# Optimization experiments

Measured on AMD Instinct MI355X. Metric: run time of the kernel, lower is better.

Reference implementation:

```python
import jax, jax.numpy as jnp
import numpy as np


def setup_inputs() -> dict:
    key = jax.random.key(0)
    kq, kk, kv = jax.random.split(key, 3)
    B, L, S, H, E = 4, 2048, 2048, 16, 64
    queries = jax.random.normal(kq, (B, L, H, E), dtype=jnp.float32)
    keys = jax.random.normal(kk, (B, S, H, E), dtype=jnp.float32)
    values = jax.random.normal(kv, (B, S, H, E), dtype=jnp.float32)
    return {"queries": queries, "keys": keys, "values": values}


def reference(queries, keys, values):
    # queries: [b,l,h,e], keys: [b,s,h,e], values: [b,s,h,d]
    e = queries.shape[-1]
    scale = 1.0 / jnp.sqrt(jnp.asarray(e, dtype=queries.dtype))
    scores = jnp.einsum('blhe,bshe->bhls', queries, keys)  # [b,h,l,s]
    attn_map = jax.nn.softmax(scale * scores, axis=-1)
    # dropout is identity in eval/reference mode
    v = jnp.einsum('bhls,bshd->blhd', attn_map, values)  # [b,l,h,d]
    return v, attn_map
```

## Files before the change

kernel.cpp:

```cpp
#include <hip/hip_runtime.h>
#include <hip/hip_bf16.h>


typedef __attribute__((ext_vector_type(4)))  float  f32x4;
typedef __attribute__((ext_vector_type(8)))  short  short8;
typedef __attribute__((ext_vector_type(4)))  short  short4v;
typedef __attribute__((ext_vector_type(4)))  unsigned short u16x4;

__device__ __forceinline__ unsigned short bf(float x) {
  return __builtin_bit_cast(unsigned short, __float2bfloat16(x));
}

__device__ __forceinline__ float bf2f(unsigned short u) {
  return __builtin_bit_cast(float, (unsigned int)u << 16);
}

__device__ __forceinline__ unsigned short f2bf(float f) {
  unsigned int u = __builtin_bit_cast(unsigned int, f);
  return (unsigned short)((u + 0x7FFFu + ((u >> 16) & 1u)) >> 16);
}

#define MFMA16(A, Bv, C) __builtin_amdgcn_mfma_f32_16x16x32_bf16(A, Bv, C, 0, 0, 0)


__global__ __launch_bounds__(256) void conv_all(const float* __restrict__ Q,
                                                const float* __restrict__ K,
                                                const float* __restrict__ V,
                                                unsigned short* __restrict__ Qbf,
                                                unsigned short* __restrict__ Kbf,
                                                unsigned short* __restrict__ VTbf) {
  __shared__ unsigned short T[64][68];
  if (blockIdx.x < 8192) {
    int idx = blockIdx.x * 256 + threadIdx.x;
    int isK = idx >> 20;
    int rem = idx & 0xFFFFF;
    int e0 = (rem & 7) << 3;
    int h  = (rem >> 3) & 15;
    int l  = (rem >> 7) & 2047;
    int b  = rem >> 18;
    const float* src = (isK ? K : Q) + (((size_t)(b * 2048 + l)) * 16 + h) * 64 + e0;
    unsigned short* dst = (isK ? Kbf : Qbf) + (((size_t)(b * 16 + h)) * 2048 + l) * 64 + e0;
    float sc = isK ? 1.0f : 0.18033688011112042f;
    float4 a = *(const float4*)src;
    float4 c = *(const float4*)(src + 4);
    u16x4 o0 = { bf(a.x * sc), bf(a.y * sc), bf(a.z * sc), bf(a.w * sc) };
    u16x4 o1 = { bf(c.x * sc), bf(c.y * sc), bf(c.z * sc), bf(c.w * sc) };
    *(u16x4*)dst = o0;
    *(u16x4*)(dst + 4) = o1;
  } else {
    int bid = blockIdx.x - 8192;
    int sc = bid & 31, bh = bid >> 5;
    int h = bh & 15, b = bh >> 4;
    int t = threadIdx.x;
    int srow = t >> 2, d0 = (t & 3) << 4;
    const float* src = V + (((size_t)(b * 2048 + sc * 64 + srow)) * 16 + h) * 64 + d0;
    float4 v0 = *(const float4*)(src + 0);
    float4 v1 = *(const float4*)(src + 4);
    float4 v2 = *(const float4*)(src + 8);
    float4 v3 = *(const float4*)(src + 12);
    T[d0+ 0][srow]=bf(v0.x); T[d0+ 1][srow]=bf(v0.y); T[d0+ 2][srow]=bf(v0.z); T[d0+ 3][srow]=bf(v0.w);
    T[d0+ 4][srow]=bf(v1.x); T[d0+ 5][srow]=bf(v1.y); T[d0+ 6][srow]=bf(v1.z); T[d0+ 7][srow]=bf(v1.w);
    T[d0+ 8][srow]=bf(v2.x); T[d0+ 9][srow]=bf(v2.y); T[d0+10][srow]=bf(v2.z); T[d0+11][srow]=bf(v2.w);
    T[d0+12][srow]=bf(v3.x); T[d0+13][srow]=bf(v3.y); T[d0+14][srow]=bf(v3.z); T[d0+15][srow]=bf(v3.w);
    __syncthreads();
    int d = t >> 2, s0 = (t & 3) << 4;
    unsigned short* dst = VTbf + ((size_t)bh * 64 + d) * 2048 + sc * 64 + s0;
#pragma unroll
    for (int j = 0; j < 16; j += 4) {
      u16x4 x = { T[d][s0 + j], T[d][s0 + j + 1], T[d][s0 + j + 2], T[d][s0 + j + 3] };
      *(u16x4*)(dst + j) = x;
    }
  }
}


__device__ __forceinline__ void gll16(const void* g, void* l) {
  __builtin_amdgcn_global_load_lds(
      (const __attribute__((address_space(1))) unsigned int*)g,
      (__attribute__((address_space(3))) unsigned int*)l, 16, 0, 0);
}

__device__ __forceinline__ void stage16(const unsigned short* gsrc, int rowStride,
                                        unsigned short* dstRow0, int lane) {
  int rr = lane >> 3;
  int cc = ((lane & 7) ^ rr) << 3;
  gll16(gsrc + (size_t)rr * rowStride + cc,       dstRow0);
  gll16(gsrc + (size_t)(8 + rr) * rowStride + cc, dstRow0 + 8 * 64);
}

__device__ __forceinline__ short8 frag(const unsigned short* tile, int row, int colb) {
  return *(const short8*)((const char*)tile + row * 128 + (colb ^ ((row & 7) << 4)));
}

__global__ __launch_bounds__(256, 3) void attn_main(
    const unsigned short* __restrict__ Qbf, const unsigned short* __restrict__ Kbf,
    const unsigned short* __restrict__ VTbf, float* __restrict__ Og,
    float* __restrict__ Ag) {

  int wg = ((blockIdx.x & 7) << 8) | (blockIdx.x >> 3);
  int qt = wg & 31, bh = wg >> 5;
  int h = bh & 15, b = bh >> 4;

  int tid = threadIdx.x, lane = tid & 63, w = tid >> 6;
  int g = lane >> 4, r16 = lane & 15;

  __shared__ __align__(16) unsigned short Qb[64][64];
  __shared__ __align__(16) unsigned short Kb[2][64][64];
  __shared__ __align__(16) unsigned short Vb[2][64][64];
  __shared__ __align__(16) unsigned short Pb[4][16][72];

  const unsigned short* qg = Qbf + ((size_t)bh * 2048 + qt * 64 + w * 16) * 64;
  const unsigned short* kg = Kbf + (size_t)bh * 2048 * 64 + (size_t)(w * 16) * 64;
  const unsigned short* vg = VTbf + (size_t)bh * 64 * 2048 + (size_t)(w * 16) * 2048;

  stage16(qg, 64, &Qb[w * 16][0], lane);
  stage16(kg,            64, &Kb[0][w * 16][0], lane);
  stage16(kg + 4096,     64, &Kb[1][w * 16][0], lane);
  stage16(kg + 2 * 4096, 64, &Vb[0][w * 16][0], lane);
  stage16(kg + 3 * 4096, 64, &Vb[1][w * 16][0], lane);
  asm volatile("s_waitcnt vmcnt(8)" ::: "memory");
  __builtin_amdgcn_s_barrier();

  short8 qf0 = frag(&Qb[0][0], w * 16 + r16, g * 16);
  short8 qf1 = frag(&Qb[0][0], w * 16 + r16, 64 + g * 16);

  float lsum = 0.0f;
  for (int ii = 0; ii < 16; ++ii) {
    const int hi = ii & 1;
    const unsigned short* sA = hi ? &Vb[0][0][0] : &Kb[0][0][0];
    const unsigned short* sB = hi ? &Vb[1][0][0] : &Kb[1][0][0];

    if (ii < 15) {
      asm volatile("s_waitcnt vmcnt(4)" ::: "memory");
    } else {
      asm volatile("s_waitcnt vmcnt(0)" ::: "memory");
    }
    __builtin_amdgcn_s_barrier();

    f32x4 st[8];
    __builtin_amdgcn_s_setprio(1);
#pragma unroll
    for (int t = 0; t < 4; ++t) {
      short8 kf0 = frag(sA, t * 16 + r16, g * 16);
      short8 kf1 = frag(sA, t * 16 + r16, 64 + g * 16);
      f32x4 z = {0.f, 0.f, 0.f, 0.f};
      z = MFMA16(kf0, qf0, z);
      z = MFMA16(kf1, qf1, z);
      st[t] = z;
    }
#pragma unroll
    for (int t = 0; t < 4; ++t) {
      short8 kf0 = frag(sB, t * 16 + r16, g * 16);
      short8 kf1 = frag(sB, t * 16 + r16, 64 + g * 16);
      f32x4 z = {0.f, 0.f, 0.f, 0.f};
      z = MFMA16(kf0, qf0, z);
      z = MFMA16(kf1, qf1, z);
      st[t + 4] = z;
    }
    __builtin_amdgcn_s_setprio(0);

    float acc = 0.f;
#pragma unroll
    for (int t = 0; t < 8; ++t) {
      float e0 = __builtin_amdgcn_exp2f(st[t][0]) + __builtin_amdgcn_exp2f(st[t][1]);
      float e1 = __builtin_amdgcn_exp2f(st[t][2]) + __builtin_amdgcn_exp2f(st[t][3]);
      acc += e0 + e1;
    }
    lsum += acc;

    __builtin_amdgcn_s_barrier();

    if (ii < 14) {
      const unsigned short* nk = kg + (size_t)(2 * ii + 4) * 4096;
      unsigned short* dA = hi ? &Vb[0][w * 16][0] : &Kb[0][w * 16][0];
      unsigned short* dB = hi ? &Vb[1][w * 16][0] : &Kb[1][w * 16][0];
      stage16(nk,        64, dA, lane);
      stage16(nk + 4096, 64, dB, lane);
    }
  }
  lsum += __shfl_xor(lsum, 16, 64);
  lsum += __shfl_xor(lsum, 32, 64);
  float rinv = 1.0f / lsum;

  f32x4 oacc[4];
#pragma unroll
  for (int t = 0; t < 4; ++t) oacc[t] = (f32x4){0.f, 0.f, 0.f, 0.f};

  stage16(kg, 64, &Kb[0][w * 16][0], lane);
  stage16(vg, 2048, &Vb[0][w * 16][0], lane);
  asm volatile("s_waitcnt vmcnt(0)" ::: "memory");
  __builtin_amdgcn_s_barrier();
  int cur = 0;

  float* aW = Ag + ((size_t)bh * 2048 + (size_t)(qt * 64 + w * 16)) * 2048;
  const int sra = lane >> 4;
  const int src4 = (lane & 15) * 4;

  for (int ch = 0; ch < 32; ++ch) {
    if (ch < 31) {
      stage16(kg + (size_t)(ch + 1) * 4096, 64, &Kb[cur ^ 1][w * 16][0], lane);
      stage16(vg + (size_t)(ch + 1) * 64, 2048, &Vb[cur ^ 1][w * 16][0], lane);
    }
    f32x4 st[4];
    __builtin_amdgcn_s_setprio(1);
#pragma unroll
    for (int t = 0; t < 4; ++t) {
      short8 kf0 = frag(&Kb[cur][0][0], t * 16 + r16, g * 16);
      short8 kf1 = frag(&Kb[cur][0][0], t * 16 + r16, 64 + g * 16);
      f32x4 z = {0.f, 0.f, 0.f, 0.f};
      z = MFMA16(kf0, qf0, z);
      z = MFMA16(kf1, qf1, z);
      st[t] = z;
    }
    __builtin_amdgcn_s_setprio(0);

#pragma unroll
    for (int t = 0; t < 4; ++t) {
      f32x4 p;
#pragma unroll
      for (int r = 0; r < 4; ++r)
        p[r] = __builtin_amdgcn_exp2f(st[t][r]) * rinv;
      u16x4 pb = { bf(p[0]), bf(p[1]), bf(p[2]), bf(p[3]) };
      *(u16x4*)&Pb[w][r16][t * 16 + 4 * g] = pb;
    }

#pragma unroll
    for (int i = 0; i < 4; ++i) {
      int row = 4 * i + sra;
      u16x4 pb4 = *(const u16x4*)&Pb[w][row][src4];
      f32x4 o = { bf2f(pb4[0]), bf2f(pb4[1]), bf2f(pb4[2]), bf2f(pb4[3]) };
      __builtin_nontemporal_store(o, (f32x4*)(aW + (size_t)row * 2048 + ch * 64 + src4));
    }

    __builtin_amdgcn_s_setprio(1);
#pragma unroll
    for (int c = 0; c < 2; ++c) {
      short8 pa = *(const short8*)((const char*)&Pb[w][r16][0] + c * 64 + g * 16);
#pragma unroll
      for (int t = 0; t < 4; ++t) {
        short8 vf = frag(&Vb[cur][0][0], t * 16 + r16, c * 64 + g * 16);
        oacc[t] = MFMA16(pa, vf, oacc[t]);
      }
    }
    __builtin_amdgcn_s_setprio(0);

    asm volatile("s_waitcnt vmcnt(4)" ::: "memory");
    __builtin_amdgcn_s_barrier();
    cur ^= 1;
  }

  float* op = Og + (((size_t)b * 2048 + (size_t)(qt * 64 + w * 16 + 4 * g)) * 16 + h) * 64;
#pragma unroll
  for (int t = 0; t < 4; ++t)
#pragma unroll
    for (int r = 0; r < 4; ++r)
      op[(size_t)r * 1024 + t * 16 + r16] = oacc[t][r];
}


__global__ __launch_bounds__(256, 2) void attn_fused(
    const float* __restrict__ Qg, const float* __restrict__ Kg,
    const float* __restrict__ Vg, float* __restrict__ Og,
    float* __restrict__ Ag) {

  const int qt = blockIdx.x & 31;
  const int bh = blockIdx.x >> 5;
  const int h  = bh & 15;
  const int b  = bh >> 4;

  const int tid  = threadIdx.x;
  const int lane = tid & 63;
  const int w    = tid >> 6;
  const int g    = lane >> 4;
  const int r16  = lane & 15;

  __shared__ __align__(16) unsigned short Qbuf[64][72];
  __shared__ __align__(16) unsigned short Kbuf[64][72];
  __shared__ __align__(16) unsigned short VT[64][68];
  __shared__ __align__(16) unsigned short Pbuf[4][16][72];

  const size_t inbase = (size_t)b * (2048u * 1024u) + (size_t)h * 64u;
  const int q0 = qt << 6;

  const int srow = tid >> 2;
  const int sd0  = (tid & 3) << 4;

  {
    const float sc = 0.18033688011112042f;
    const float* gp = Qg + inbase + (size_t)(q0 + srow) * 1024u + sd0;
    float4 va = *(const float4*)(gp + 0);
    float4 vb = *(const float4*)(gp + 4);
    float4 vc = *(const float4*)(gp + 8);
    float4 vd = *(const float4*)(gp + 12);
    unsigned short* dst = &Qbuf[srow][sd0];
    dst[0]=f2bf(va.x*sc); dst[1]=f2bf(va.y*sc); dst[2]=f2bf(va.z*sc); dst[3]=f2bf(va.w*sc);
    dst[4]=f2bf(vb.x*sc); dst[5]=f2bf(vb.y*sc); dst[6]=f2bf(vb.z*sc); dst[7]=f2bf(vb.w*sc);
    dst[8]=f2bf(vc.x*sc); dst[9]=f2bf(vc.y*sc); dst[10]=f2bf(vc.z*sc); dst[11]=f2bf(vc.w*sc);
    dst[12]=f2bf(vd.x*sc); dst[13]=f2bf(vd.y*sc); dst[14]=f2bf(vd.z*sc); dst[15]=f2bf(vd.w*sc);
  }
  __syncthreads();

  const short8 qf0 = *(const short8*)&Qbuf[w*16 + r16][g*8];
  const short8 qf1 = *(const short8*)&Qbuf[w*16 + r16][32 + g*8];

  f32x4 mrow = { -3e38f, -3e38f, -3e38f, -3e38f };
  f32x4 lrow = { 0.f, 0.f, 0.f, 0.f };

  for (int ch = 0; ch < 32; ++ch) {
    __syncthreads();
    {
      const float* gp = Kg + inbase + (size_t)(ch*64 + srow) * 1024u + sd0;
      float4 va = *(const float4*)(gp + 0);
      float4 vb = *(const float4*)(gp + 4);
      float4 vc = *(const float4*)(gp + 8);
      float4 vd = *(const float4*)(gp + 12);
      unsigned short* dst = &Kbuf[srow][sd0];
      dst[0]=f2bf(va.x); dst[1]=f2bf(va.y); dst[2]=f2bf(va.z); dst[3]=f2bf(va.w);
      dst[4]=f2bf(vb.x); dst[5]=f2bf(vb.y); dst[6]=f2bf(vb.z); dst[7]=f2bf(vb.w);
      dst[8]=f2bf(vc.x); dst[9]=f2bf(vc.y); dst[10]=f2bf(vc.z); dst[11]=f2bf(vc.w);
      dst[12]=f2bf(vd.x); dst[13]=f2bf(vd.y); dst[14]=f2bf(vd.z); dst[15]=f2bf(vd.w);
    }
    __syncthreads();

    f32x4 st[4];
#pragma unroll
    for (int t = 0; t < 4; ++t) {
      const short8 kf0 = *(const short8*)&Kbuf[t*16 + r16][g*8];
      const short8 kf1 = *(const short8*)&Kbuf[t*16 + r16][32 + g*8];
      f32x4 z = {0.f, 0.f, 0.f, 0.f};
      z = MFMA16(qf0, kf0, z);
      z = MFMA16(qf1, kf1, z);
      st[t] = z;
    }

    f32x4 cm = st[0];
#pragma unroll
    for (int t = 1; t < 4; ++t)
#pragma unroll
      for (int r = 0; r < 4; ++r) cm[r] = fmaxf(cm[r], st[t][r]);
#pragma unroll
    for (int i = 1; i < 16; i <<= 1)
#pragma unroll
      for (int r = 0; r < 4; ++r) cm[r] = fmaxf(cm[r], __shfl_xor(cm[r], i, 64));

    f32x4 mn, corr, sum = {0.f, 0.f, 0.f, 0.f};
#pragma unroll
    for (int r = 0; r < 4; ++r) {
      mn[r]   = fmaxf(mrow[r], cm[r]);
      corr[r] = exp2f(mrow[r] - mn[r]);
    }
#pragma unroll
    for (int t = 0; t < 4; ++t)
#pragma unroll
      for (int r = 0; r < 4; ++r) sum[r] += exp2f(st[t][r] - mn[r]);
#pragma unroll
    for (int i = 1; i < 16; i <<= 1)
#pragma unroll
      for (int r = 0; r < 4; ++r) sum[r] += __shfl_xor(sum[r], i, 64);
#pragma unroll
    for (int r = 0; r < 4; ++r) {
      lrow[r] = lrow[r] * corr[r] + sum[r];
      mrow[r] = mn[r];
    }
  }

  f32x4 rinv;
#pragma unroll
  for (int r = 0; r < 4; ++r) rinv[r] = 1.0f / lrow[r];

  f32x4 oacc[4];
#pragma unroll
  for (int t = 0; t < 4; ++t) oacc[t] = (f32x4){0.f, 0.f, 0.f, 0.f};

  float* aRow = Ag + ((size_t)bh * 2048u + (size_t)(q0 + w*16 + 4*g)) * 2048u;

  for (int ch = 0; ch < 32; ++ch) {
    __syncthreads();
    {
      const float* gp = Kg + inbase + (size_t)(ch*64 + srow) * 1024u + sd0;
      float4 va = *(const float4*)(gp + 0);
      float4 vb = *(const float4*)(gp + 4);
      float4 vc = *(const float4*)(gp + 8);
      float4 vd = *(const float4*)(gp + 12);
      unsigned short* dst = &Kbuf[srow][sd0];
      dst[0]=f2bf(va.x); dst[1]=f2bf(va.y); dst[2]=f2bf(va.z); dst[3]=f2bf(va.w);
      dst[4]=f2bf(vb.x); dst[5]=f2bf(vb.y); dst[6]=f2bf(vb.z); dst[7]=f2bf(vb.w);
      dst[8]=f2bf(vc.x); dst[9]=f2bf(vc.y); dst[10]=f2bf(vc.z); dst[11]=f2bf(vc.w);
      dst[12]=f2bf(vd.x); dst[13]=f2bf(vd.y); dst[14]=f2bf(vd.z); dst[15]=f2bf(vd.w);
    }
    {
      const float* gp = Vg + inbase + (size_t)(ch*64 + lane) * 1024u + (size_t)(w*16);
      float4 va = *(const float4*)(gp + 0);
      float4 vb = *(const float4*)(gp + 4);
      float4 vc = *(const float4*)(gp + 8);
      float4 vd = *(const float4*)(gp + 12);
      const int dbase = w * 16;
      VT[dbase+ 0][lane]=f2bf(va.x); VT[dbase+ 1][lane]=f2bf(va.y);
      VT[dbase+ 2][lane]=f2bf(va.z); VT[dbase+ 3][lane]=f2bf(va.w);
      VT[dbase+ 4][lane]=f2bf(vb.x); VT[dbase+ 5][lane]=f2bf(vb.y);
      VT[dbase+ 6][lane]=f2bf(vb.z); VT[dbase+ 7][lane]=f2bf(vb.w);
      VT[dbase+ 8][lane]=f2bf(vc.x); VT[dbase+ 9][lane]=f2bf(vc.y);
      VT[dbase+10][lane]=f2bf(vc.z); VT[dbase+11][lane]=f2bf(vc.w);
      VT[dbase+12][lane]=f2bf(vd.x); VT[dbase+13][lane]=f2bf(vd.y);
      VT[dbase+14][lane]=f2bf(vd.z); VT[dbase+15][lane]=f2bf(vd.w);
    }
    __syncthreads();

    f32x4 st[4];
#pragma unroll
    for (int t = 0; t < 4; ++t) {
      const short8 kf0 = *(const short8*)&Kbuf[t*16 + r16][g*8];
      const short8 kf1 = *(const short8*)&Kbuf[t*16 + r16][32 + g*8];
      f32x4 z = {0.f, 0.f, 0.f, 0.f};
      z = MFMA16(qf0, kf0, z);
      z = MFMA16(qf1, kf1, z);
      st[t] = z;
    }

#pragma unroll
    for (int t = 0; t < 4; ++t) {
#pragma unroll
      for (int r = 0; r < 4; ++r) {
        float p = exp2f(st[t][r] - mrow[r]) * rinv[r];
        aRow[(size_t)r * 2048u + (size_t)(ch*64 + t*16 + r16)] = p;
        Pbuf[w][4*g + r][t*16 + r16] = f2bf(p);
      }
    }

#pragma unroll
    for (int c = 0; c < 2; ++c) {
      const short8 pa = *(const short8*)&Pbuf[w][r16][c*32 + g*8];
#pragma unroll
      for (int t = 0; t < 4; ++t) {
        const unsigned short* vp = &VT[t*16 + r16][c*32 + g*8];
        short4v lo = *(const short4v*)vp;
        short4v hi = *(const short4v*)(vp + 4);
        short8 vbf = { lo[0], lo[1], lo[2], lo[3], hi[0], hi[1], hi[2], hi[3] };
        oacc[t] = MFMA16(pa, vbf, oacc[t]);
      }
    }
  }

  float* op = Og + (((size_t)b * 2048u + (size_t)(q0 + w*16 + 4*g)) * 16u + (size_t)h) * 64u;
#pragma unroll
  for (int t = 0; t < 4; ++t)
#pragma unroll
    for (int r = 0; r < 4; ++r)
      op[(size_t)r * 1024u + (size_t)(t*16 + r16)] = oacc[t][r];
}


extern "C" void kernel_launch(void* const* d_in, const int* in_sizes, int n_in,
                              void* d_out, int out_size, void* d_ws, size_t ws_size,
                              hipStream_t stream) {
  const float* Q = (const float*)d_in[0];
  const float* K = (const float*)d_in[1];
  const float* V = (const float*)d_in[2];
  float* Og = (float*)d_out;
  float* Ag = (float*)d_out + 8388608;

  const size_t NEED = 3ull * 8388608ull * 2ull;
  if (ws_size >= NEED) {
    unsigned short* Qbf  = (unsigned short*)d_ws;
    unsigned short* Kbf  = Qbf + 8388608;
    unsigned short* VTbf = Kbf + 8388608;
    conv_all<<<dim3(10240), dim3(256), 0, stream>>>(Q, K, V, Qbf, Kbf, VTbf);
    attn_main<<<dim3(2048), dim3(256), 0, stream>>>(Qbf, Kbf, VTbf, Og, Ag);
  } else {
    attn_fused<<<dim3(2048), dim3(256), 0, stream>>>(Q, K, V, Og, Ag);
  }
}
```

Measured before the change: 246.2 us.

## Use 128-row query tiles with 8 waves and convert Q in-kernel

```diff
diff --git a/kernel.cpp b/kernel.cpp
--- a/kernel.cpp
+++ b/kernel.cpp
@@ -23,32 +23,27 @@
 #define MFMA16(A, Bv, C) __builtin_amdgcn_mfma_f32_16x16x32_bf16(A, Bv, C, 0, 0, 0)
 
 
-__global__ __launch_bounds__(256) void conv_all(const float* __restrict__ Q,
-                                                const float* __restrict__ K,
+__global__ __launch_bounds__(256) void conv_all(const float* __restrict__ K,
                                                 const float* __restrict__ V,
-                                                unsigned short* __restrict__ Qbf,
                                                 unsigned short* __restrict__ Kbf,
                                                 unsigned short* __restrict__ VTbf) {
   __shared__ unsigned short T[64][68];
-  if (blockIdx.x < 8192) {
+  if (blockIdx.x < 4096) {
     int idx = blockIdx.x * 256 + threadIdx.x;
-    int isK = idx >> 20;
-    int rem = idx & 0xFFFFF;
-    int e0 = (rem & 7) << 3;
-    int h  = (rem >> 3) & 15;
-    int l  = (rem >> 7) & 2047;
-    int b  = rem >> 18;
-    const float* src = (isK ? K : Q) + (((size_t)(b * 2048 + l)) * 16 + h) * 64 + e0;
-    unsigned short* dst = (isK ? Kbf : Qbf) + (((size_t)(b * 16 + h)) * 2048 + l) * 64 + e0;
-    float sc = isK ? 1.0f : 0.18033688011112042f;
+    int e0 = (idx & 7) << 3;
+    int h  = (idx >> 3) & 15;
+    int l  = (idx >> 7) & 2047;
+    int b  = idx >> 18;
+    const float* src = K + (((size_t)(b * 2048 + l)) * 16 + h) * 64 + e0;
+    unsigned short* dst = Kbf + (((size_t)(b * 16 + h)) * 2048 + l) * 64 + e0;
     float4 a = *(const float4*)src;
     float4 c = *(const float4*)(src + 4);
-    u16x4 o0 = { bf(a.x * sc), bf(a.y * sc), bf(a.z * sc), bf(a.w * sc) };
-    u16x4 o1 = { bf(c.x * sc), bf(c.y * sc), bf(c.z * sc), bf(c.w * sc) };
+    u16x4 o0 = { bf(a.x), bf(a.y), bf(a.z), bf(a.w) };
+    u16x4 o1 = { bf(c.x), bf(c.y), bf(c.z), bf(c.w) };
     *(u16x4*)dst = o0;
     *(u16x4*)(dst + 4) = o1;
   } else {
-    int bid = blockIdx.x - 8192;
+    int bid = blockIdx.x - 4096;
     int sc = bid & 31, bh = bid >> 5;
     int h = bh & 15, b = bh >> 4;
     int t = threadIdx.x;
@@ -80,58 +75,72 @@
       (__attribute__((address_space(3))) unsigned int*)l, 16, 0, 0);
 }
 
-__device__ __forceinline__ void stage16(const unsigned short* gsrc, int rowStride,
-                                        unsigned short* dstRow0, int lane) {
+__device__ __forceinline__ void stage8(const unsigned short* gsrc, int rowStride,
+                                       unsigned short* dstRow0, int lane) {
   int rr = lane >> 3;
   int cc = ((lane & 7) ^ rr) << 3;
-  gll16(gsrc + (size_t)rr * rowStride + cc,       dstRow0);
-  gll16(gsrc + (size_t)(8 + rr) * rowStride + cc, dstRow0 + 8 * 64);
+  gll16(gsrc + (size_t)rr * rowStride + cc, dstRow0);
 }
 
 __device__ __forceinline__ short8 frag(const unsigned short* tile, int row, int colb) {
   return *(const short8*)((const char*)tile + row * 128 + (colb ^ ((row & 7) << 4)));
 }
 
-__global__ __launch_bounds__(256, 3) void attn_main(
-    const unsigned short* __restrict__ Qbf, const unsigned short* __restrict__ Kbf,
+__global__ __launch_bounds__(512, 2) void attn_main(
+    const float* __restrict__ Qf, const unsigned short* __restrict__ Kbf,
     const unsigned short* __restrict__ VTbf, float* __restrict__ Og,
     float* __restrict__ Ag) {
 
-  int wg = ((blockIdx.x & 7) << 8) | (blockIdx.x >> 3);
-  int qt = wg & 31, bh = wg >> 5;
+  int wg = ((blockIdx.x & 7) << 7) | (blockIdx.x >> 3);
+  int qt = wg & 15, bh = wg >> 4;
   int h = bh & 15, b = bh >> 4;
 
   int tid = threadIdx.x, lane = tid & 63, w = tid >> 6;
   int g = lane >> 4, r16 = lane & 15;
-
-  __shared__ __align__(16) unsigned short Qb[64][64];
+  int q0 = qt * 128;
+
+  __shared__ __align__(16) unsigned short Qb[128][64];
   __shared__ __align__(16) unsigned short Kb[2][64][64];
   __shared__ __align__(16) unsigned short Vb[2][64][64];
-  __shared__ __align__(16) unsigned short Pb[4][16][72];
-
-  const unsigned short* qg = Qbf + ((size_t)bh * 2048 + qt * 64 + w * 16) * 64;
-  const unsigned short* kg = Kbf + (size_t)bh * 2048 * 64 + (size_t)(w * 16) * 64;
-  const unsigned short* vg = VTbf + (size_t)bh * 64 * 2048 + (size_t)(w * 16) * 2048;
-
-  stage16(qg, 64, &Qb[w * 16][0], lane);
-  stage16(kg,            64, &Kb[0][w * 16][0], lane);
-  stage16(kg + 4096,     64, &Kb[1][w * 16][0], lane);
-  stage16(kg + 2 * 4096, 64, &Vb[0][w * 16][0], lane);
-  stage16(kg + 3 * 4096, 64, &Vb[1][w * 16][0], lane);
-  asm volatile("s_waitcnt vmcnt(8)" ::: "memory");
+  __shared__ __align__(16) unsigned short Pb[8][16][72];
+
+  const unsigned short* kg = Kbf + (size_t)bh * 2048 * 64 + (size_t)(w * 8) * 64;
+  const unsigned short* vg = VTbf + (size_t)bh * 64 * 2048 + (size_t)(w * 8) * 2048;
+
+  {
+    const float sc = 0.18033688011112042f;
+    int row = tid >> 2, c0 = (tid & 3) << 4;
+    const float* qsrc = Qf + (((size_t)(b * 2048 + q0 + row)) * 16 + h) * 64 + c0;
+    float4 qa = *(const float4*)(qsrc + 0);
+    float4 qb = *(const float4*)(qsrc + 4);
+    float4 qc = *(const float4*)(qsrc + 8);
+    float4 qd = *(const float4*)(qsrc + 12);
+    stage8(kg,            64, &Kb[0][w * 8][0], lane);
+    stage8(kg + 4096,     64, &Kb[1][w * 8][0], lane);
+    stage8(kg + 2 * 4096, 64, &Vb[0][w * 8][0], lane);
+    stage8(kg + 3 * 4096, 64, &Vb[1][w * 8][0], lane);
+    unsigned short* qdst = &Qb[row][c0];
+    u16x4 o0 = { bf(qa.x*sc), bf(qa.y*sc), bf(qa.z*sc), bf(qa.w*sc) };
+    u16x4 o1 = { bf(qb.x*sc), bf(qb.y*sc), bf(qb.z*sc), bf(qb.w*sc) };
+    u16x4 o2 = { bf(qc.x*sc), bf(qc.y*sc), bf(qc.z*sc), bf(qc.w*sc) };
+    u16x4 o3 = { bf(qd.x*sc), bf(qd.y*sc), bf(qd.z*sc), bf(qd.w*sc) };
+    *(u16x4*)(qdst + 0) = o0;  *(u16x4*)(qdst + 4)  = o1;
+    *(u16x4*)(qdst + 8) = o2;  *(u16x4*)(qdst + 12) = o3;
+  }
+  asm volatile("s_waitcnt lgkmcnt(0)" ::: "memory");
   __builtin_amdgcn_s_barrier();
 
-  short8 qf0 = frag(&Qb[0][0], w * 16 + r16, g * 16);
-  short8 qf1 = frag(&Qb[0][0], w * 16 + r16, 64 + g * 16);
+  short8 qf0 = *(const short8*)((const char*)&Qb[w * 16 + r16][0] + g * 16);
+  short8 qf1 = *(const short8*)((const char*)&Qb[w * 16 + r16][0] + 64 + g * 16);
 
   float lsum = 0.0f;
   for (int ii = 0; ii < 16; ++ii) {
-    const int hi = ii & 1;
-    const unsigned short* sA = hi ? &Vb[0][0][0] : &Kb[0][0][0];
-    const unsigned short* sB = hi ? &Vb[1][0][0] : &Kb[1][0][0];
+    const int hsel = ii & 1;
+    const unsigned short* sA = hsel ? &Vb[0][0][0] : &Kb[0][0][0];
+    const unsigned short* sB = hsel ? &Vb[1][0][0] : &Kb[1][0][0];
 
     if (ii < 15) {
-      asm volatile("s_waitcnt vmcnt(4)" ::: "memory");
+      asm volatile("s_waitcnt vmcnt(2)" ::: "memory");
     } else {
       asm volatile("s_waitcnt vmcnt(0)" ::: "memory");
     }
@@ -172,10 +181,10 @@
 
     if (ii < 14) {
       const unsigned short* nk = kg + (size_t)(2 * ii + 4) * 4096;
-      unsigned short* dA = hi ? &Vb[0][w * 16][0] : &Kb[0][w * 16][0];
-      unsigned short* dB = hi ? &Vb[1][w * 16][0] : &Kb[1][w * 16][0];
-      stage16(nk,        64, dA, lane);
-      stage16(nk + 4096, 64, dB, lane);
+      unsigned short* dA = hsel ? &Vb[0][w * 8][0] : &Kb[0][w * 8][0];
+      unsigned short* dB = hsel ? &Vb[1][w * 8][0] : &Kb[1][w * 8][0];
+      stage8(nk,        64, dA, lane);
+      stage8(nk + 4096, 64, dB, lane);
     }
   }
   lsum += __shfl_xor(lsum, 16, 64);
@@ -186,20 +195,20 @@
 #pragma unroll
   for (int t = 0; t < 4; ++t) oacc[t] = (f32x4){0.f, 0.f, 0.f, 0.f};
 
-  stage16(kg, 64, &Kb[0][w * 16][0], lane);
-  stage16(vg, 2048, &Vb[0][w * 16][0], lane);
+  stage8(kg, 64, &Kb[0][w * 8][0], lane);
+  stage8(vg, 2048, &Vb[0][w * 8][0], lane);
   asm volatile("s_waitcnt vmcnt(0)" ::: "memory");
   __builtin_amdgcn_s_barrier();
   int cur = 0;
 
-  float* aW = Ag + ((size_t)bh * 2048 + (size_t)(qt * 64 + w * 16)) * 2048;
+  float* aW = Ag + ((size_t)bh * 2048 + (size_t)(q0 + w * 16)) * 2048;
   const int sra = lane >> 4;
   const int src4 = (lane & 15) * 4;
 
   for (int ch = 0; ch < 32; ++ch) {
     if (ch < 31) {
-      stage16(kg + (size_t)(ch + 1) * 4096, 64, &Kb[cur ^ 1][w * 16][0], lane);
-      stage16(vg + (size_t)(ch + 1) * 64, 2048, &Vb[cur ^ 1][w * 16][0], lane);
+      stage8(kg + (size_t)(ch + 1) * 4096, 64, &Kb[cur ^ 1][w * 8][0], lane);
+      stage8(vg + (size_t)(ch + 1) * 64, 2048, &Vb[cur ^ 1][w * 8][0], lane);
     }
     f32x4 st[4];
     __builtin_amdgcn_s_setprio(1);
@@ -249,7 +258,7 @@
     cur ^= 1;
   }
 
-  float* op = Og + (((size_t)b * 2048 + (size_t)(qt * 64 + w * 16 + 4 * g)) * 16 + h) * 64;
+  float* op = Og + (((size_t)b * 2048 + (size_t)(q0 + w * 16 + 4 * g)) * 16 + h) * 64;
 #pragma unroll
   for (int t = 0; t < 4; ++t)
 #pragma unroll
@@ -459,13 +468,12 @@
   float* Og = (float*)d_out;
   float* Ag = (float*)d_out + 8388608;
 
-  const size_t NEED = 3ull * 8388608ull * 2ull;
+  const size_t NEED = 2ull * 8388608ull * 2ull;
   if (ws_size >= NEED) {
-    unsigned short* Qbf  = (unsigned short*)d_ws;
-    unsigned short* Kbf  = Qbf + 8388608;
+    unsigned short* Kbf  = (unsigned short*)d_ws;
     unsigned short* VTbf = Kbf + 8388608;
-    conv_all<<<dim3(10240), dim3(256), 0, stream>>>(Q, K, V, Qbf, Kbf, VTbf);
-    attn_main<<<dim3(2048), dim3(256), 0, stream>>>(Qbf, Kbf, VTbf, Og, Ag);
+    conv_all<<<dim3(6144), dim3(256), 0, stream>>>(K, V, Kbf, VTbf);
+    attn_main<<<dim3(1024), dim3(512), 0, stream>>>(Q, Kbf, VTbf, Og, Ag);
   } else {
     attn_fused<<<dim3(2048), dim3(256), 0, stream>>>(Q, K, V, Og, Ag);
   }
```

Result: faster. 237.5 us (-3.5%).
